# Optimization experiments

Hardware: AMD Instinct MI355X
Metric: run time of the kernel (lower is better)

## Reference

```python
import jax, jax.numpy as jnp
import numpy as np
from jax.ops import segment_sum

N_NODES = 1_000_000
N_EDGES = 10_000_000


def gcn_conv(x, W, b, src, dst, n_nodes):
    """PyG GCNConv: add self-loops, sym-normalize, linear, scatter-sum, bias."""
    h = x @ W  # [N, out]
    loop = jnp.arange(n_nodes, dtype=src.dtype)
    s = jnp.concatenate([src, loop])  # sources incl. self-loops
    d = jnp.concatenate([dst, loop])  # targets incl. self-loops
    deg = segment_sum(jnp.ones(s.shape[0], dtype=h.dtype), d, num_segments=n_nodes)
    dinv = jnp.where(deg > 0, jax.lax.rsqrt(deg), 0.0)  # deg^-1/2, 0 for isolated
    norm = dinv[s] * dinv[d]  # [E+N]
    msg = h[s] * norm[:, None]  # gather + scale
    out = segment_sum(msg, d, num_segments=n_nodes)  # scatter-add at targets
    return out + b


def setup_inputs() -> dict:
    key = jax.random.key(0)
    k1, k2, k3, k4, k5 = jax.random.split(key, 5)
    x = jax.random.normal(k1, (N_NODES, 3), dtype=jnp.float32)
    edge_index = jax.random.randint(k2, (2, N_EDGES), 0, N_NODES, dtype=jnp.int64)
    # Glorot-ish init for the two GCNConv layers (3->8, 8->2) with bias
    W1 = jax.random.normal(k3, (3, 8), dtype=jnp.float32) * (1.0 / np.sqrt(3.0))
    b1 = jnp.zeros((8,), dtype=jnp.float32)
    W2 = jax.random.normal(k4, (8, 2), dtype=jnp.float32) * (1.0 / np.sqrt(8.0))
    b2 = jnp.zeros((2,), dtype=jnp.float32)
    return {"x": x, "edge_index": edge_index, "W1": W1, "b1": b1, "W2": W2, "b2": b2}


def reference(x, edge_index, W1, b1, W2, b2):
    src, dst = edge_index[0], edge_index[1]
    n = x.shape[0]
    h = gcn_conv(x, W1, b1, src, dst, n)
    h = jax.nn.relu(h)
    return gcn_conv(h, W2, b2, src, dst, n)
```

## Files before the change

kernel.cpp:

```cpp
#include <hip/hip_runtime.h>


#define BSH 12
#define BKT 4096
#define NBKT_MAX 256
#define CAP 43008
#define TILE 16384
#define MSB 1024
#define AGB 512

typedef unsigned uvec4 __attribute__((ext_vector_type(4)));

__device__ inline unsigned bf16r(float f) {
    unsigned u = __float_as_uint(f);
    return (u + 0x7FFFu + ((u >> 16) & 1u)) & 0xFFFF0000u;
}
__device__ inline unsigned pack2(float a, float b) {
    return (bf16r(a) >> 16) | (bf16r(b) & 0xFFFF0000u);
}
__device__ inline float unp(unsigned w, int half) {
    return half ? __uint_as_float(w & 0xFFFF0000u) : __uint_as_float(w << 16);
}

__device__ inline void xq_dec(unsigned u, float& v0, float& v1, float& v2) {
    float sc = __uint_as_float((((u >> 27) & 31u) + 104u) << 23);
    v0 = (float)(((int)(u << 5)) >> 23) * sc;
    v1 = (float)(((int)(u << 14)) >> 23) * sc;
    v2 = (float)(((int)(u << 23)) >> 23) * sc;
}

__global__ void k_init(int* __restrict__ bcur, int nbkt) {
    int t = threadIdx.x;
    if (t < nbkt) bcur[t] = t * CAP;
}

__global__ void k_msplit(const int* __restrict__ src, const int* __restrict__ dst,
                         int* __restrict__ bcur, unsigned* __restrict__ esort, int e) {
    __shared__ unsigned stage[TILE];
    __shared__ unsigned char bid[TILE];
    __shared__ int h[NBKT_MAX];
    __shared__ int lscan[NBKT_MAX];
    __shared__ int baseadj[NBKT_MAX];
    int t = threadIdx.x;
    int base = blockIdx.x * TILE;
    int cnt = min(TILE, e - base);
    if (t < NBKT_MAX) h[t] = 0;
    __syncthreads();

    unsigned val[16];
    int bk[16], rnk[16];
#pragma unroll
    for (int k = 0; k < 16; ++k) {
        int i = base + k * MSB + t;
        bk[k] = -1;
        if (i < e) {
            int d = __builtin_nontemporal_load(&dst[i]);
            int s = __builtin_nontemporal_load(&src[i]);
            bk[k] = d >> BSH;
            val[k] = ((unsigned)(d & (BKT - 1)) << 20) | (unsigned)s;
            rnk[k] = atomicAdd(&h[bk[k]], 1);
        }
    }
    __syncthreads();
    int c = (t < NBKT_MAX) ? h[t] : 0;
    __syncthreads();
    if (t < NBKT_MAX) lscan[t] = c;
    __syncthreads();
    for (int off = 1; off < NBKT_MAX; off <<= 1) {
        int w = (t < NBKT_MAX && t >= off) ? lscan[t - off] : 0;
        __syncthreads();
        if (t < NBKT_MAX) lscan[t] += w;
        __syncthreads();
    }
    int ex = (t < NBKT_MAX) ? (lscan[t] - c) : 0;
    __syncthreads();
    if (t < NBKT_MAX) {
        lscan[t] = ex;
        if (c > 0) baseadj[t] = atomicAdd(&bcur[t], c) - ex;
    }
    __syncthreads();

#pragma unroll
    for (int k = 0; k < 16; ++k) {
        if (bk[k] >= 0) {
            int idx = lscan[bk[k]] + rnk[k];
            stage[idx] = val[k];
            bid[idx] = (unsigned char)bk[k];
        }
    }
    __syncthreads();
#pragma unroll
    for (int k = 0; k < 16; ++k) {
        int j = k * MSB + t;
        if (j < cnt) esort[baseadj[bid[j]] + j] = stage[j];
    }
}

__global__ void k_deg_xd(const unsigned* __restrict__ esort, const int* __restrict__ bcur,
                         const float* __restrict__ x,
                         unsigned* __restrict__ xq, float* __restrict__ dinv, int n) {
    __shared__ int deg[BKT];
    int b = blockIdx.x, t = threadIdx.x;
#pragma unroll
    for (int k = 0; k < BKT / AGB; ++k) deg[k * AGB + t] = 0;
    __syncthreads();
    int beg = b * CAP, end = bcur[b];
    int m = end - beg;
    int ng = (m + 3) >> 2;
    for (int g = t; g < ng; g += AGB) {
        int p = beg + g * 4;
        uvec4 v = __builtin_nontemporal_load((const uvec4*)(esort + p));
        int lim = end - p;
        if (lim > 0) atomicAdd(&deg[v.x >> 20], 1);
        if (lim > 1) atomicAdd(&deg[v.y >> 20], 1);
        if (lim > 2) atomicAdd(&deg[v.z >> 20], 1);
        if (lim > 3) atomicAdd(&deg[v.w >> 20], 1);
    }
    __syncthreads();
#pragma unroll
    for (int k = 0; k < BKT / AGB; ++k) {
        int dl = k * AGB + t;
        int node = (b << BSH) + dl;
        if (node >= n) continue;
        float di = rsqrtf((float)deg[dl] + 1.0f);
        float v0 = x[3 * node] * di, v1 = x[3 * node + 1] * di, v2 = x[3 * node + 2] * di;
        dinv[node] = di;
        float mx = fmaxf(fmaxf(fabsf(v0), fabsf(v1)), fabsf(v2));
        int ee;
        frexpf(mx, &ee);
        ee = min(max(ee, -15), 16);
        float sc = exp2f((float)(8 - ee));
        int m0 = min(max(__float2int_rn(v0 * sc), -256), 255);
        int m1 = min(max(__float2int_rn(v1 * sc), -256), 255);
        int m2 = min(max(__float2int_rn(v2 * sc), -256), 255);
        xq[node] = ((unsigned)(ee + 15) << 27) |
                   ((unsigned)(m0 & 0x1FF) << 18) |
                   ((unsigned)(m1 & 0x1FF) << 9) |
                   (unsigned)(m2 & 0x1FF);
    }
}

__global__ void k_l1a(const unsigned* __restrict__ esort, const int* __restrict__ bcur,
                      const unsigned* __restrict__ xq, unsigned* __restrict__ part1) {
    __shared__ float acc[BKT * 3];
    int bid = blockIdx.x, b = bid >> 1, hh = bid & 1;
    int t = threadIdx.x;
#pragma unroll
    for (int k = 0; k < BKT * 3 / AGB; ++k) acc[k * AGB + t] = 0.0f;
    __syncthreads();
    int beg = b * CAP, end = bcur[b];
    int m = end - beg;
    int half = (((m + 1) >> 1) + 7) & ~7;
    int s0 = beg + hh * half;
    int e0 = min(end, s0 + half);
    int mh = e0 - s0;
    int ng = (mh + 7) >> 3;
    for (int g = t; g < ng; g += AGB) {
        int p = s0 + g * 8;
        uvec4 va = *(const uvec4*)(esort + p);
        uvec4 vb = *(const uvec4*)(esort + p + 4);
        unsigned ed[8] = { va.x, va.y, va.z, va.w, vb.x, vb.y, vb.z, vb.w };
        int lim = e0 - p;
        unsigned u[8];
#pragma unroll
        for (int j = 0; j < 8; ++j)
            u[j] = (j < lim) ? xq[ed[j] & 0xFFFFFu] : 0u;
#pragma unroll
        for (int j = 0; j < 8; ++j) {
            if (j < lim) {
                float s0f, s1f, s2f;
                xq_dec(u[j], s0f, s1f, s2f);
                int q = ed[j] >> 20;
                atomicAdd(&acc[q * 3 + 0], s0f);
                atomicAdd(&acc[q * 3 + 1], s1f);
                atomicAdd(&acc[q * 3 + 2], s2f);
            }
        }
    }
    __syncthreads();
    unsigned* pb = part1 + (size_t)bid * 6144;
#pragma unroll
    for (int j = 0; j < 3; ++j)
        for (int i = t; i < 2048; i += AGB)
            pb[j * 2048 + i] = pack2(acc[(2 * i) * 3 + j], acc[(2 * i + 1) * 3 + j]);
}

__global__ void k_l1b(const unsigned* __restrict__ part1, const unsigned* __restrict__ xq,
                      const float* __restrict__ dinv,
                      const float* __restrict__ W1, const float* __restrict__ b1,
                      const float* __restrict__ W2, unsigned* __restrict__ g2, int n) {
    int b = blockIdx.x, t = threadIdx.x;
    const unsigned* pa = part1 + (size_t)(2 * b) * 6144;
    const unsigned* pbv = part1 + (size_t)(2 * b + 1) * 6144;
#pragma unroll
    for (int k = 0; k < BKT / AGB; ++k) {
        int dl = k * AGB + t;
        int node = (b << BSH) + dl;
        if (node >= n) continue;
        int i = dl >> 1, hf = dl & 1;
        float a[3];
#pragma unroll
        for (int j = 0; j < 3; ++j)
            a[j] = unp(pa[j * 2048 + i], hf) + unp(pbv[j * 2048 + i], hf);
        float s0, s1, s2;
        xq_dec(xq[node], s0, s1, s2);
        float di = dinv[node];
        float a0 = (a[0] + s0) * di;
        float a1 = (a[1] + s1) * di;
        float a2 = (a[2] + s2) * di;
        float h0 = 0.0f, h1 = 0.0f;
#pragma unroll
        for (int j = 0; j < 8; ++j) {
            float r = fmaxf(a0 * W1[j] + a1 * W1[8 + j] + a2 * W1[16 + j] + b1[j], 0.0f);
            h0 += r * W2[2 * j + 0];
            h1 += r * W2[2 * j + 1];
        }
        g2[node] = (bf16r(h0 * di) >> 16) | bf16r(h1 * di);
    }
}

__global__ void k_l2a(const unsigned* __restrict__ esort, const int* __restrict__ bcur,
                      const unsigned* __restrict__ g2, unsigned* __restrict__ part2) {
    __shared__ float acc[BKT * 2];
    int bid = blockIdx.x, b = bid >> 1, hh = bid & 1;
    int t = threadIdx.x;
#pragma unroll
    for (int k = 0; k < BKT * 2 / AGB; ++k) acc[k * AGB + t] = 0.0f;
    __syncthreads();
    int beg = b * CAP, end = bcur[b];
    int m = end - beg;
    int half = (((m + 1) >> 1) + 7) & ~7;
    int s0 = beg + hh * half;
    int e0 = min(end, s0 + half);
    int mh = e0 - s0;
    int ng = (mh + 7) >> 3;
    for (int g = t; g < ng; g += AGB) {
        int p = s0 + g * 8;
        uvec4 va = *(const uvec4*)(esort + p);
        uvec4 vb = *(const uvec4*)(esort + p + 4);
        unsigned ed[8] = { va.x, va.y, va.z, va.w, vb.x, vb.y, vb.z, vb.w };
        int lim = e0 - p;
        unsigned u[8];
#pragma unroll
        for (int j = 0; j < 8; ++j)
            u[j] = (j < lim) ? g2[ed[j] & 0xFFFFFu] : 0u;
#pragma unroll
        for (int j = 0; j < 8; ++j) {
            if (j < lim) {
                int q = ed[j] >> 20;
                atomicAdd(&acc[q * 2 + 0], __uint_as_float(u[j] << 16));
                atomicAdd(&acc[q * 2 + 1], __uint_as_float(u[j] & 0xFFFF0000u));
            }
        }
    }
    __syncthreads();
    unsigned* pb = part2 + (size_t)bid * 4096;
#pragma unroll
    for (int j = 0; j < 2; ++j)
        for (int i = t; i < 2048; i += AGB)
            pb[j * 2048 + i] = pack2(acc[(2 * i) * 2 + j], acc[(2 * i + 1) * 2 + j]);
}

__global__ void k_l2b(const unsigned* __restrict__ part2, const unsigned* __restrict__ g2,
                      const float* __restrict__ dinv, const float* __restrict__ b2,
                      float2* __restrict__ out, int n) {
    int b = blockIdx.x, t = threadIdx.x;
    const unsigned* pa = part2 + (size_t)(2 * b) * 4096;
    const unsigned* pbv = part2 + (size_t)(2 * b + 1) * 4096;
#pragma unroll
    for (int k = 0; k < BKT / AGB; ++k) {
        int dl = k * AGB + t;
        int node = (b << BSH) + dl;
        if (node >= n) continue;
        int i = dl >> 1, hf = dl & 1;
        float a0 = unp(pa[i], hf) + unp(pbv[i], hf);
        float a1 = unp(pa[2048 + i], hf) + unp(pbv[2048 + i], hf);
        unsigned gg = g2[node];
        float s0 = __uint_as_float(gg << 16);
        float s1 = __uint_as_float(gg & 0xFFFF0000u);
        float di = dinv[node];
        out[node] = make_float2((a0 + s0) * di + b2[0], (a1 + s1) * di + b2[1]);
    }
}

extern "C" void kernel_launch(void* const* d_in, const int* in_sizes, int n_in,
                              void* d_out, int out_size, void* d_ws, size_t ws_size,
                              hipStream_t stream) {
    const float* x  = (const float*)d_in[0];
    const int*   ei = (const int*)d_in[1];
    const float* W1 = (const float*)d_in[2];
    const float* b1 = (const float*)d_in[3];
    const float* W2 = (const float*)d_in[4];
    const float* b2 = (const float*)d_in[5];
    float2* out = (float2*)d_out;

    const int n = in_sizes[0] / 3;
    const int e = in_sizes[1] / 2;
    const int* src = ei;
    const int* dst = ei + e;
    const int nbkt = (n + BKT - 1) >> BSH;

    char* w = (char*)d_ws;
    unsigned* xq    = (unsigned*)w;  w += (size_t)n * sizeof(unsigned);
    float*    dinv  = (float*)w;     w += (size_t)n * sizeof(float);
    unsigned* g2    = (unsigned*)w;  w += (size_t)n * sizeof(unsigned);
    unsigned* esort = (unsigned*)w;  w += ((size_t)nbkt * CAP + 64) * sizeof(unsigned);
    int*      bcur  = (int*)w;       w += 1024 * sizeof(int);
    unsigned* part  = (unsigned*)w;

    const int nb_ms = (e + TILE - 1) / TILE;

    k_init  <<<1, 256, 0, stream>>>(bcur, nbkt);
    k_msplit<<<nb_ms, MSB, 0, stream>>>(src, dst, bcur, esort, e);
    k_deg_xd<<<nbkt, AGB, 0, stream>>>(esort, bcur, x, xq, dinv, n);
    k_l1a   <<<nbkt * 2, AGB, 0, stream>>>(esort, bcur, xq, part);
    k_l1b   <<<nbkt, AGB, 0, stream>>>(part, xq, dinv, W1, b1, W2, g2, n);
    k_l2a   <<<nbkt * 2, AGB, 0, stream>>>(esort, bcur, g2, part);
    k_l2b   <<<nbkt, AGB, 0, stream>>>(part, g2, dinv, b2, out, n);
}
```

Measured before the change: 379.6 us.

## Bin edges by source window and stage node features in LDS for aggregation

The degree pass now also builds, per bucket half, a histogram of edges by source window. Both aggregation kernels use it to counting-sort their edges into LDS by source window. Each block then loops over all source windows, loading a 4096-node slice of the quantized features into LDS and gathering from there instead of doing random global loads. This trades scattered global or L2 gathers for per-window cooperative loads and two barriers per window, plus a much larger LDS footprint that limits occupancy.

New measurement: 1.021 ms. +169.0%, slower.

```diff
diff --git a/kernel.cpp b/kernel.cpp
--- a/kernel.cpp
+++ b/kernel.cpp
@@ -8,6 +8,9 @@
 #define TILE 16384
 #define MSB 1024
 #define AGB 512
+#define EHALF 21504
+#define NWIN 256
+#define WSH 12
 
 typedef unsigned uvec4 __attribute__((ext_vector_type(4)));
 
@@ -21,7 +24,6 @@
 __device__ inline float unp(unsigned w, int half) {
     return half ? __uint_as_float(w & 0xFFFF0000u) : __uint_as_float(w << 16);
 }
-
 __device__ inline void xq_dec(unsigned u, float& v0, float& v1, float& v2) {
     float sc = __uint_as_float((((u >> 27) & 31u) + 104u) << 23);
     v0 = (float)(((int)(u << 5)) >> 23) * sc;
@@ -97,26 +99,36 @@
 }
 
 __global__ void k_deg_xd(const unsigned* __restrict__ esort, const int* __restrict__ bcur,
-                         const float* __restrict__ x,
-                         unsigned* __restrict__ xq, float* __restrict__ dinv, int n) {
+                         const float* __restrict__ x, unsigned* __restrict__ xq,
+                         float* __restrict__ dinv, int* __restrict__ winhist, int n) {
     __shared__ int deg[BKT];
+    __shared__ int winh[2 * NWIN];
     int b = blockIdx.x, t = threadIdx.x;
 #pragma unroll
     for (int k = 0; k < BKT / AGB; ++k) deg[k * AGB + t] = 0;
+    winh[t] = 0;
     __syncthreads();
     int beg = b * CAP, end = bcur[b];
     int m = end - beg;
+    int half = (((m + 1) >> 1) + 7) & ~7;
     int ng = (m + 3) >> 2;
     for (int g = t; g < ng; g += AGB) {
-        int p = beg + g * 4;
+        int off = g * 4;
+        int p = beg + off;
         uvec4 v = __builtin_nontemporal_load((const uvec4*)(esort + p));
+        int hh = (off >= half) ? 1 : 0;
         int lim = end - p;
-        if (lim > 0) atomicAdd(&deg[v.x >> 20], 1);
-        if (lim > 1) atomicAdd(&deg[v.y >> 20], 1);
-        if (lim > 2) atomicAdd(&deg[v.z >> 20], 1);
-        if (lim > 3) atomicAdd(&deg[v.w >> 20], 1);
-    }
-    __syncthreads();
+        unsigned ed[4] = { v.x, v.y, v.z, v.w };
+#pragma unroll
+        for (int j = 0; j < 4; ++j) {
+            if (j < lim) {
+                atomicAdd(&deg[ed[j] >> 20], 1);
+                atomicAdd(&winh[hh * NWIN + ((ed[j] & 0xFFFFFu) >> WSH)], 1);
+            }
+        }
+    }
+    __syncthreads();
+    winhist[(b << 9) + t] = winh[t];
 #pragma unroll
     for (int k = 0; k < BKT / AGB; ++k) {
         int dl = k * AGB + t;
@@ -141,43 +153,65 @@
 }
 
 __global__ void k_l1a(const unsigned* __restrict__ esort, const int* __restrict__ bcur,
-                      const unsigned* __restrict__ xq, unsigned* __restrict__ part1) {
+                      const int* __restrict__ winhist, const unsigned* __restrict__ xq,
+                      unsigned* __restrict__ part1, int nwin) {
+    __shared__ unsigned eds[EHALF];
     __shared__ float acc[BKT * 3];
+    __shared__ unsigned stg[4096];
+    __shared__ int wb[NWIN + 1];
+    __shared__ int wcur[NWIN];
     int bid = blockIdx.x, b = bid >> 1, hh = bid & 1;
     int t = threadIdx.x;
 #pragma unroll
     for (int k = 0; k < BKT * 3 / AGB; ++k) acc[k * AGB + t] = 0.0f;
+    int c = (t < NWIN) ? winhist[(b << 9) + (hh << 8) + t] : 0;
+    if (t < NWIN) wcur[t] = c;
+    __syncthreads();
+    for (int off = 1; off < NWIN; off <<= 1) {
+        int v = (t < NWIN && t >= off) ? wcur[t - off] : 0;
+        __syncthreads();
+        if (t < NWIN) wcur[t] += v;
+        __syncthreads();
+    }
+    if (t < NWIN) {
+        int inc = wcur[t];
+        wb[t] = inc - c;
+        if (t == NWIN - 1) wb[NWIN] = inc;
+    }
+    __syncthreads();
+    if (t < NWIN) wcur[t] = wb[t];
     __syncthreads();
     int beg = b * CAP, end = bcur[b];
     int m = end - beg;
     int half = (((m + 1) >> 1) + 7) & ~7;
     int s0 = beg + hh * half;
     int e0 = min(end, s0 + half);
-    int mh = e0 - s0;
-    int ng = (mh + 7) >> 3;
-    for (int g = t; g < ng; g += AGB) {
-        int p = s0 + g * 8;
-        uvec4 va = *(const uvec4*)(esort + p);
-        uvec4 vb = *(const uvec4*)(esort + p + 4);
-        unsigned ed[8] = { va.x, va.y, va.z, va.w, vb.x, vb.y, vb.z, vb.w };
-        int lim = e0 - p;
-        unsigned u[8];
-#pragma unroll
-        for (int j = 0; j < 8; ++j)
-            u[j] = (j < lim) ? xq[ed[j] & 0xFFFFFu] : 0u;
-#pragma unroll
-        for (int j = 0; j < 8; ++j) {
-            if (j < lim) {
-                float s0f, s1f, s2f;
-                xq_dec(u[j], s0f, s1f, s2f);
-                int q = ed[j] >> 20;
-                atomicAdd(&acc[q * 3 + 0], s0f);
-                atomicAdd(&acc[q * 3 + 1], s1f);
-                atomicAdd(&acc[q * 3 + 2], s2f);
-            }
-        }
-    }
-    __syncthreads();
+    for (int p = s0 + t; p < e0; p += AGB) {
+        unsigned v = __builtin_nontemporal_load(&esort[p]);
+        int w = (v & 0xFFFFFu) >> WSH;
+        int pos = atomicAdd(&wcur[w], 1);
+        eds[pos] = v;
+    }
+    __syncthreads();
+    for (int w = 0; w < nwin; ++w) {
+        int rb = wb[w], re = wb[w + 1];
+        if (rb == re) continue;
+        const uvec4* xs = (const uvec4*)(xq + (w << WSH));
+        ((uvec4*)stg)[t] = xs[t];
+        ((uvec4*)stg)[t + AGB] = xs[t + AGB];
+        __syncthreads();
+        for (int r = rb + t; r < re; r += AGB) {
+            unsigned v = eds[r];
+            int srcl = v & (BKT - 1);
+            int q = v >> 20;
+            float s0f, s1f, s2f;
+            xq_dec(stg[srcl], s0f, s1f, s2f);
+            atomicAdd(&acc[q * 3 + 0], s0f);
+            atomicAdd(&acc[q * 3 + 1], s1f);
+            atomicAdd(&acc[q * 3 + 2], s2f);
+        }
+        __syncthreads();
+    }
     unsigned* pb = part1 + (size_t)bid * 6144;
 #pragma unroll
     for (int j = 0; j < 3; ++j)
@@ -220,40 +254,62 @@
 }
 
 __global__ void k_l2a(const unsigned* __restrict__ esort, const int* __restrict__ bcur,
-                      const unsigned* __restrict__ g2, unsigned* __restrict__ part2) {
+                      const int* __restrict__ winhist, const unsigned* __restrict__ g2,
+                      unsigned* __restrict__ part2, int nwin) {
+    __shared__ unsigned eds[EHALF];
     __shared__ float acc[BKT * 2];
+    __shared__ unsigned stg[4096];
+    __shared__ int wb[NWIN + 1];
+    __shared__ int wcur[NWIN];
     int bid = blockIdx.x, b = bid >> 1, hh = bid & 1;
     int t = threadIdx.x;
 #pragma unroll
     for (int k = 0; k < BKT * 2 / AGB; ++k) acc[k * AGB + t] = 0.0f;
+    int c = (t < NWIN) ? winhist[(b << 9) + (hh << 8) + t] : 0;
+    if (t < NWIN) wcur[t] = c;
+    __syncthreads();
+    for (int off = 1; off < NWIN; off <<= 1) {
+        int v = (t < NWIN && t >= off) ? wcur[t - off] : 0;
+        __syncthreads();
+        if (t < NWIN) wcur[t] += v;
+        __syncthreads();
+    }
+    if (t < NWIN) {
+        int inc = wcur[t];
+        wb[t] = inc - c;
+        if (t == NWIN - 1) wb[NWIN] = inc;
+    }
+    __syncthreads();
+    if (t < NWIN) wcur[t] = wb[t];
     __syncthreads();
     int beg = b * CAP, end = bcur[b];
     int m = end - beg;
     int half = (((m + 1) >> 1) + 7) & ~7;
     int s0 = beg + hh * half;
     int e0 = min(end, s0 + half);
-    int mh = e0 - s0;
-    int ng = (mh + 7) >> 3;
-    for (int g = t; g < ng; g += AGB) {
-        int p = s0 + g * 8;
-        uvec4 va = *(const uvec4*)(esort + p);
-        uvec4 vb = *(const uvec4*)(esort + p + 4);
-        unsigned ed[8] = { va.x, va.y, va.z, va.w, vb.x, vb.y, vb.z, vb.w };
-        int lim = e0 - p;
-        unsigned u[8];
-#pragma unroll
-        for (int j = 0; j < 8; ++j)
-            u[j] = (j < lim) ? g2[ed[j] & 0xFFFFFu] : 0u;
-#pragma unroll
-        for (int j = 0; j < 8; ++j) {
-            if (j < lim) {
-                int q = ed[j] >> 20;
-                atomicAdd(&acc[q * 2 + 0], __uint_as_float(u[j] << 16));
-                atomicAdd(&acc[q * 2 + 1], __uint_as_float(u[j] & 0xFFFF0000u));
-            }
-        }
-    }
-    __syncthreads();
+    for (int p = s0 + t; p < e0; p += AGB) {
+        unsigned v = __builtin_nontemporal_load(&esort[p]);
+        int w = (v & 0xFFFFFu) >> WSH;
+        int pos = atomicAdd(&wcur[w], 1);
+        eds[pos] = v;
+    }
+    __syncthreads();
+    for (int w = 0; w < nwin; ++w) {
+        int rb = wb[w], re = wb[w + 1];
+        if (rb == re) continue;
+        const uvec4* gs = (const uvec4*)(g2 + (w << WSH));
+        ((uvec4*)stg)[t] = gs[t];
+        ((uvec4*)stg)[t + AGB] = gs[t + AGB];
+        __syncthreads();
+        for (int r = rb + t; r < re; r += AGB) {
+            unsigned v = eds[r];
+            unsigned gg = stg[v & (BKT - 1)];
+            int q = v >> 20;
+            atomicAdd(&acc[q * 2 + 0], __uint_as_float(gg << 16));
+            atomicAdd(&acc[q * 2 + 1], __uint_as_float(gg & 0xFFFF0000u));
+        }
+        __syncthreads();
+    }
     unsigned* pb = part2 + (size_t)bid * 4096;
 #pragma unroll
     for (int j = 0; j < 2; ++j)
@@ -299,22 +355,24 @@
     const int* src = ei;
     const int* dst = ei + e;
     const int nbkt = (n + BKT - 1) >> BSH;
+    const int nwin = nbkt;
 
     char* w = (char*)d_ws;
-    unsigned* xq    = (unsigned*)w;  w += (size_t)n * sizeof(unsigned);
-    float*    dinv  = (float*)w;     w += (size_t)n * sizeof(float);
-    unsigned* g2    = (unsigned*)w;  w += (size_t)n * sizeof(unsigned);
-    unsigned* esort = (unsigned*)w;  w += ((size_t)nbkt * CAP + 64) * sizeof(unsigned);
-    int*      bcur  = (int*)w;       w += 1024 * sizeof(int);
-    unsigned* part  = (unsigned*)w;
+    unsigned* xq      = (unsigned*)w;  w += (size_t)n * sizeof(unsigned);
+    float*    dinv    = (float*)w;     w += (size_t)n * sizeof(float);
+    unsigned* g2      = (unsigned*)w;  w += (size_t)n * sizeof(unsigned);
+    unsigned* esort   = (unsigned*)w;  w += ((size_t)nbkt * CAP + 64) * sizeof(unsigned);
+    int*      bcur    = (int*)w;       w += 1024 * sizeof(int);
+    int*      winhist = (int*)w;       w += (size_t)nbkt * 512 * sizeof(int);
+    unsigned* part    = (unsigned*)w;
 
     const int nb_ms = (e + TILE - 1) / TILE;
 
     k_init  <<<1, 256, 0, stream>>>(bcur, nbkt);
     k_msplit<<<nb_ms, MSB, 0, stream>>>(src, dst, bcur, esort, e);
-    k_deg_xd<<<nbkt, AGB, 0, stream>>>(esort, bcur, x, xq, dinv, n);
-    k_l1a   <<<nbkt * 2, AGB, 0, stream>>>(esort, bcur, xq, part);
+    k_deg_xd<<<nbkt, AGB, 0, stream>>>(esort, bcur, x, xq, dinv, winhist, n);
+    k_l1a   <<<nbkt * 2, AGB, 0, stream>>>(esort, bcur, winhist, xq, part, nwin);
     k_l1b   <<<nbkt, AGB, 0, stream>>>(part, xq, dinv, W1, b1, W2, g2, n);
-    k_l2a   <<<nbkt * 2, AGB, 0, stream>>>(esort, bcur, g2, part);
+    k_l2a   <<<nbkt * 2, AGB, 0, stream>>>(esort, bcur, winhist, g2, part, nwin);
     k_l2b   <<<nbkt, AGB, 0, stream>>>(part, g2, dinv, b2, out, n);
 }
```
